# Optimization experiments

Hardware: AMD Instinct MI355X
Metric: run time of the kernel (lower is better)

## Reference

```python
import jax, jax.numpy as jnp
import numpy as np

N_NODES = 50000
N_EDGES = 800000
HIDDEN = 128
UNIFIED = 128


def _sage_conv(x, src, dst, W_l, b_l, W_r, n_nodes):
    # PyG SAGEConv (mean aggr): out = lin_l(mean_{j in N(i)} x_j) + lin_r(x_i)
    msgs = x[src]  # [E, d] gather of source-node features
    agg = jax.ops.segment_sum(msgs, dst, num_segments=n_nodes)  # [N, d]
    cnt = jax.ops.segment_sum(jnp.ones((src.shape[0],), dtype=x.dtype), dst,
                              num_segments=n_nodes)
    agg = agg / jnp.maximum(cnt, 1.0)[:, None]  # mean; isolated nodes -> 0
    return agg @ W_l.T + b_l + x @ W_r.T


def setup_inputs() -> dict:
    key = jax.random.key(0)
    ks = jax.random.split(key, 8)
    s = 1.0 / np.sqrt(HIDDEN)
    x = jax.random.normal(ks[0], (N_NODES, HIDDEN), dtype=jnp.float32)
    edge_index = jax.random.randint(ks[1], (2, N_EDGES), 0, N_NODES, dtype=jnp.int64)
    W1_l = jax.random.normal(ks[2], (HIDDEN, HIDDEN), dtype=jnp.float32) * s
    b1_l = jnp.zeros((HIDDEN,), dtype=jnp.float32)
    W1_r = jax.random.normal(ks[3], (HIDDEN, HIDDEN), dtype=jnp.float32) * s
    W2_l = jax.random.normal(ks[4], (UNIFIED, HIDDEN), dtype=jnp.float32) * s
    b2_l = jnp.zeros((UNIFIED,), dtype=jnp.float32)
    W2_r = jax.random.normal(ks[5], (UNIFIED, HIDDEN), dtype=jnp.float32) * s
    return {"x": x, "edge_index": edge_index,
            "W1_l": W1_l, "b1_l": b1_l, "W1_r": W1_r,
            "W2_l": W2_l, "b2_l": b2_l, "W2_r": W2_r}


def reference(x, edge_index, W1_l, b1_l, W1_r, W2_l, b2_l, W2_r):
    src, dst = edge_index[0], edge_index[1]
    n = x.shape[0]
    h = jax.nn.relu(_sage_conv(x, src, dst, W1_l, b1_l, W1_r, n))
    return _sage_conv(h, src, dst, W2_l, b2_l, W2_r, n)
```

## Files before the change

### kernel.cpp

```cpp
#include <hip/hip_runtime.h>

#define N_NODES 50000
#define HIDDEN 128
#define NBUCK ((N_NODES + 127) >> 7)

typedef __attribute__((ext_vector_type(8))) short short8;
typedef __attribute__((ext_vector_type(4))) float f32x4;

__device__ __forceinline__ unsigned short f2bf(float f) {
    union { float f; unsigned int u; } a; a.f = f;
    unsigned int u = a.u;
    u += 0x7FFFu + ((u >> 16) & 1u);
    return (unsigned short)(u >> 16);
}
__device__ __forceinline__ float bf2f(unsigned int bits16) {
    union { unsigned int u; float f; } a; a.u = bits16 << 16;
    return a.f;
}

__global__ __launch_bounds__(256) void pack_both(
    const float* __restrict__ W1l, const float* __restrict__ W1r,
    const float* __restrict__ W2l, const float* __restrict__ W2r,
    unsigned short* __restrict__ Wp1, unsigned short* __restrict__ Wp2,
    int* __restrict__ bcnt) {
    int tid = blockIdx.x * blockDim.x + threadIdx.x;
    if (tid < NBUCK) bcnt[tid] = 0;
    const int which = tid >> 15;
    const int t2 = tid & 32767;
    int j = t2 & 7, lane = (t2 >> 3) & 63, nf = (t2 >> 9) & 7, ks = t2 >> 12;
    int k = ks * 32 + ((lane >> 4) * 8) + j;
    int t = nf * 16 + (lane & 15);
    const float* Wl = which ? W2l : W1l;
    const float* Wr = which ? W2r : W1r;
    float v = (k < 128) ? Wl[t * 128 + k] : Wr[t * 128 + (k - 128)];
    (which ? Wp2 : Wp1)[t2] = f2bf(v);
}

__global__ void cast_bf16(const float* __restrict__ x, unsigned short* __restrict__ xb, int n4) {
    int i = blockIdx.x * blockDim.x + threadIdx.x;
    if (i >= n4) return;
    float4 v = reinterpret_cast<const float4*>(x)[i];
    ushort4 o = make_ushort4(f2bf(v.x), f2bf(v.y), f2bf(v.z), f2bf(v.w));
    reinterpret_cast<ushort4*>(xb)[i] = o;
}


__global__ __launch_bounds__(1024) void bucket_hist(const int* __restrict__ dst, int E,
                                                    int* __restrict__ bcnt) {
    __shared__ int h[NBUCK];
    for (int i = threadIdx.x; i < NBUCK; i += 1024) h[i] = 0;
    __syncthreads();
    for (int e = blockIdx.x * 1024 + threadIdx.x; e < E; e += gridDim.x * 1024)
        atomicAdd(&h[dst[e] >> 7], 1);
    __syncthreads();
    for (int i = threadIdx.x; i < NBUCK; i += 1024)
        if (h[i]) atomicAdd(&bcnt[i], h[i]);
}

__global__ __launch_bounds__(512) void scan_buckets(const int* __restrict__ bcnt,
                                                    int* __restrict__ boff,
                                                    int* __restrict__ bcur) {
    __shared__ int ws[8];
    const int tid = threadIdx.x, lane = tid & 63, wid = tid >> 6;
    const int v = (tid < NBUCK) ? bcnt[tid] : 0;
    int incl = v;
#pragma unroll
    for (int off = 1; off < 64; off <<= 1) {
        int t = __shfl_up(incl, off);
        if (lane >= off) incl += t;
    }
    if (lane == 63) ws[wid] = incl;
    __syncthreads();
    if (wid == 0) {
        int wv = (lane < 8) ? ws[lane] : 0;
        int wincl = wv;
#pragma unroll
        for (int off = 1; off < 8; off <<= 1) {
            int t = __shfl_up(wincl, off);
            if (lane >= off) wincl += t;
        }
        if (lane < 8) ws[lane] = wincl - wv;
    }
    __syncthreads();
    const int excl = ws[wid] + incl - v;
    if (tid < NBUCK) { boff[tid] = excl; bcur[tid] = excl; }
    if (tid == NBUCK - 1) boff[NBUCK] = excl + v;
}

#define PCHUNK 4096
__global__ __launch_bounds__(1024) void partition_edges(
    const int* __restrict__ src, const int* __restrict__ dst, int E,
    int* __restrict__ bcur, unsigned int* __restrict__ packed) {
    __shared__ int h[NBUCK];
    __shared__ int base[NBUCK];
    const int tid = threadIdx.x;
    const int c0 = blockIdx.x * PCHUNK;
    for (int i = tid; i < NBUCK; i += 1024) h[i] = 0;
    __syncthreads();

    unsigned int val[4];
    int bk[4];
#pragma unroll
    for (int u = 0; u < 4; ++u) {
        const int e = c0 + u * 1024 + tid;
        if (e < E) {
            const int d = dst[e];
            val[u] = ((unsigned int)d << 16) | (unsigned int)src[e];
            bk[u] = d >> 7;
            atomicAdd(&h[bk[u]], 1);
        } else {
            bk[u] = -1;
        }
    }
    __syncthreads();
    for (int i = tid; i < NBUCK; i += 1024) {
        base[i] = h[i] ? atomicAdd(&bcur[i], h[i]) : 0;
        h[i] = 0;
    }
    __syncthreads();
#pragma unroll
    for (int u = 0; u < 4; ++u) {
        if (bk[u] >= 0) {
            const int pos = base[bk[u]] + atomicAdd(&h[bk[u]], 1);
            packed[pos] = val[u];
        }
    }
}

__global__ __launch_bounds__(256) void build_rows(const unsigned int* __restrict__ packed,
                                                  const int* __restrict__ boff,
                                                  int* __restrict__ row_start,
                                                  unsigned short* __restrict__ ssrc) {
    __shared__ int lh[128];
    __shared__ int lc[128];
    __shared__ int htot;
    const int b = blockIdx.x;
    const int gbase = boff[b], gend = boff[b + 1];
    const int tid = threadIdx.x;
    if (tid < 128) lh[tid] = 0;
    __syncthreads();
    for (int i = gbase + tid; i < gend; i += 256)
        atomicAdd(&lh[(packed[i] >> 16) & 127], 1);
    __syncthreads();
    int v = 0, incl = 0;
    if (tid < 128) {
        const int lane = tid & 63;
        v = lh[tid];
        incl = v;
#pragma unroll
        for (int off = 1; off < 64; off <<= 1) {
            int t = __shfl_up(incl, off);
            if (lane >= off) incl += t;
        }
        if (tid == 63) htot = incl;
    }
    __syncthreads();
    if (tid < 128) {
        const int excl = incl - v + ((tid >= 64) ? htot : 0);
        lc[tid] = gbase + excl;
        const int node = b * 128 + tid;
        if (node <= N_NODES) row_start[node] = gbase + excl;
    }
    __syncthreads();
    for (int i = gbase + tid; i < gend; i += 256) {
        const unsigned int p = packed[i];
        const int pos = atomicAdd(&lc[(p >> 16) & 127], 1);
        ssrc[pos] = (unsigned short)(p & 0xffffu);
    }
}

__global__ __launch_bounds__(256) void aggregate_mean_bf16(
    const unsigned short* __restrict__ featb, const int* __restrict__ row_start,
    const unsigned short* __restrict__ ssrc, unsigned short* __restrict__ aggb) {
    const int node = blockIdx.x * 8 + (threadIdx.x >> 5);
    const int l = threadIdx.x & 31;
    if (node >= N_NODES) return;
    const int beg = row_start[node], end = row_start[node + 1];
    float acc[4][4];
#pragma unroll
    for (int u = 0; u < 4; ++u)
#pragma unroll
        for (int f = 0; f < 4; ++f) acc[u][f] = 0.f;

    int j = beg;
    for (; j + 3 < end; j += 4) {
#pragma unroll
        for (int u = 0; u < 4; ++u) {
            const int s = ssrc[j + u];
            const ushort4 v = *reinterpret_cast<const ushort4*>(&featb[(size_t)s * HIDDEN + 4 * l]);
            acc[u][0] += bf2f(v.x); acc[u][1] += bf2f(v.y);
            acc[u][2] += bf2f(v.z); acc[u][3] += bf2f(v.w);
        }
    }
    for (; j < end; ++j) {
        const int s = ssrc[j];
        const ushort4 v = *reinterpret_cast<const ushort4*>(&featb[(size_t)s * HIDDEN + 4 * l]);
        acc[0][0] += bf2f(v.x); acc[0][1] += bf2f(v.y);
        acc[0][2] += bf2f(v.z); acc[0][3] += bf2f(v.w);
    }
    const int d = end - beg;
    const float inv = d ? 1.0f / (float)d : 0.0f;
    ushort4 o;
    o.x = f2bf((acc[0][0] + acc[1][0] + acc[2][0] + acc[3][0]) * inv);
    o.y = f2bf((acc[0][1] + acc[1][1] + acc[2][1] + acc[3][1]) * inv);
    o.z = f2bf((acc[0][2] + acc[1][2] + acc[2][2] + acc[3][2]) * inv);
    o.w = f2bf((acc[0][3] + acc[1][3] + acc[2][3] + acc[3][3]) * inv);
    *reinterpret_cast<ushort4*>(&aggb[(size_t)node * HIDDEN + 4 * l]) = o;
}

template <int WRITE_BF16_RELU>
__global__ __launch_bounds__(256) void mfma_linear(
    const unsigned short* aggb, const unsigned short* xb,
    const unsigned short* __restrict__ Wp, const float* __restrict__ bias,
    unsigned short* out_b, float* out_f) {
    const int lane = threadIdx.x & 63;
    const int wave = threadIdx.x >> 6;
    const int wm = wave >> 1, wn = wave & 1;
    const int rowbase = blockIdx.x * 64 + wm * 32;
    const int colbase = wn * 64;
    const int l15 = lane & 15, l4 = lane >> 4;

    f32x4 acc[2][4];
#pragma unroll
    for (int m = 0; m < 2; ++m)
#pragma unroll
        for (int nf = 0; nf < 4; ++nf) acc[m][nf] = (f32x4){0.f, 0.f, 0.f, 0.f};

#pragma unroll
    for (int ks = 0; ks < 8; ++ks) {
        const unsigned short* Asrc = (ks < 4) ? aggb : xb;
        const int koff = (ks & 3) * 32 + l4 * 8;
        short8 a[2];
#pragma unroll
        for (int m = 0; m < 2; ++m) {
            int row = rowbase + m * 16 + l15;
            if (row >= N_NODES) row = N_NODES - 1;
            a[m] = *reinterpret_cast<const short8*>(&Asrc[(size_t)row * HIDDEN + koff]);
        }
#pragma unroll
        for (int nf = 0; nf < 4; ++nf) {
            const int nfg = (colbase >> 4) + nf;
            short8 b = *reinterpret_cast<const short8*>(&Wp[(((size_t)ks * 8 + nfg) * 64 + lane) * 8]);
            acc[0][nf] = __builtin_amdgcn_mfma_f32_16x16x32_bf16(a[0], b, acc[0][nf], 0, 0, 0);
            acc[1][nf] = __builtin_amdgcn_mfma_f32_16x16x32_bf16(a[1], b, acc[1][nf], 0, 0, 0);
        }
    }

#pragma unroll
    for (int nf = 0; nf < 4; ++nf) {
        const int col = colbase + nf * 16 + l15;
        const float bv = bias[col];
#pragma unroll
        for (int m = 0; m < 2; ++m) {
#pragma unroll
            for (int r = 0; r < 4; ++r) {
                const int row = rowbase + m * 16 + l4 * 4 + r;
                if (row < N_NODES) {
                    float v = acc[m][nf][r] + bv;
                    if (WRITE_BF16_RELU) {
                        v = fmaxf(v, 0.0f);
                        out_b[(size_t)row * HIDDEN + col] = f2bf(v);
                    } else {
                        out_f[(size_t)row * HIDDEN + col] = v;
                    }
                }
            }
        }
    }
}

extern "C" void kernel_launch(void* const* d_in, const int* in_sizes, int n_in,
                              void* d_out, int out_size, void* d_ws, size_t ws_size,
                              hipStream_t stream) {
    const float* x   = (const float*)d_in[0];
    const int*   ei  = (const int*)d_in[1];
    const float* W1l = (const float*)d_in[2];
    const float* b1  = (const float*)d_in[3];
    const float* W1r = (const float*)d_in[4];
    const float* W2l = (const float*)d_in[5];
    const float* b2  = (const float*)d_in[6];
    const float* W2r = (const float*)d_in[7];

    const int E = in_sizes[1] / 2;
    const int* src = ei;
    const int* dst = ei + E;

    int* iws        = (int*)d_ws;
    int* bcnt       = iws;
    int* boff       = iws + 400;
    int* bcur       = iws + 800;
    int* row_start  = iws + 1200;
    unsigned int* packed = (unsigned int*)(iws + 51204);
    unsigned short* ssrc = (unsigned short*)(iws + 51204 + E);
    unsigned short* xb   = ssrc + E;
    unsigned short* aggb = xb + (size_t)N_NODES * HIDDEN;
    unsigned short* Wp1  = aggb + (size_t)N_NODES * HIDDEN;
    unsigned short* Wp2  = Wp1 + 256 * HIDDEN;

    pack_both<<<256, 256, 0, stream>>>(W1l, W1r, W2l, W2r, Wp1, Wp2, bcnt);
    cast_bf16<<<(N_NODES * HIDDEN / 4 + 255) / 256, 256, 0, stream>>>(x, xb, N_NODES * HIDDEN / 4);

    bucket_hist<<<196, 1024, 0, stream>>>(dst, E, bcnt);
    scan_buckets<<<1, 512, 0, stream>>>(bcnt, boff, bcur);
    partition_edges<<<(E + PCHUNK - 1) / PCHUNK, 1024, 0, stream>>>(src, dst, E, bcur, packed);
    build_rows<<<NBUCK, 256, 0, stream>>>(packed, boff, row_start, ssrc);

    const int aggGrid = (N_NODES + 7) / 8;
    const int linGrid = (N_NODES + 63) / 64;

    aggregate_mean_bf16<<<aggGrid, 256, 0, stream>>>(xb, row_start, ssrc, aggb);
    mfma_linear<1><<<linGrid, 256, 0, stream>>>(aggb, xb, Wp1, b1, xb, nullptr);

    aggregate_mean_bf16<<<aggGrid, 256, 0, stream>>>(xb, row_start, ssrc, aggb);
    mfma_linear<0><<<linGrid, 256, 0, stream>>>(aggb, xb, Wp2, b2, nullptr, (float*)d_out);
}
```

Measured before the change: 152.5 us.

## Fuse neighbor mean aggregation into MFMA linear kernel via swizzled shared memory

Each 64-node block first gathers and averages its neighbors' bf16 features into an XOR-swizzled shared-memory tile, then runs the MFMA linear layer reading the aggregated half from LDS and the self half from global. This removes the separate aggregation kernel and the global write and read of the aggregated buffer per layer. Layer 1 now writes its output to a separate buffer instead of overwriting xb, which avoids a race between blocks. Fewer waves now cover the gather (16 lanes per node, 4 nodes per wave in sequence), which may reduce latency hiding. A leftover dummy load of featb[0] is dead code that the compiler should remove.

```diff
diff --git a/kernel.cpp b/kernel.cpp
--- a/kernel.cpp
+++ b/kernel.cpp
@@ -169,54 +169,65 @@
     }
 }
 
-__global__ __launch_bounds__(256) void aggregate_mean_bf16(
-    const unsigned short* __restrict__ featb, const int* __restrict__ row_start,
-    const unsigned short* __restrict__ ssrc, unsigned short* __restrict__ aggb) {
-    const int node = blockIdx.x * 8 + (threadIdx.x >> 5);
-    const int l = threadIdx.x & 31;
-    if (node >= N_NODES) return;
-    const int beg = row_start[node], end = row_start[node + 1];
-    float acc[4][4];
-#pragma unroll
-    for (int u = 0; u < 4; ++u)
-#pragma unroll
-        for (int f = 0; f < 4; ++f) acc[u][f] = 0.f;
-
-    int j = beg;
-    for (; j + 3 < end; j += 4) {
-#pragma unroll
-        for (int u = 0; u < 4; ++u) {
-            const int s = ssrc[j + u];
-            const ushort4 v = *reinterpret_cast<const ushort4*>(&featb[(size_t)s * HIDDEN + 4 * l]);
-            acc[u][0] += bf2f(v.x); acc[u][1] += bf2f(v.y);
-            acc[u][2] += bf2f(v.z); acc[u][3] += bf2f(v.w);
-        }
-    }
-    for (; j < end; ++j) {
-        const int s = ssrc[j];
-        const ushort4 v = *reinterpret_cast<const ushort4*>(&featb[(size_t)s * HIDDEN + 4 * l]);
-        acc[0][0] += bf2f(v.x); acc[0][1] += bf2f(v.y);
-        acc[0][2] += bf2f(v.z); acc[0][3] += bf2f(v.w);
-    }
-    const int d = end - beg;
-    const float inv = d ? 1.0f / (float)d : 0.0f;
-    ushort4 o;
-    o.x = f2bf((acc[0][0] + acc[1][0] + acc[2][0] + acc[3][0]) * inv);
-    o.y = f2bf((acc[0][1] + acc[1][1] + acc[2][1] + acc[3][1]) * inv);
-    o.z = f2bf((acc[0][2] + acc[1][2] + acc[2][2] + acc[3][2]) * inv);
-    o.w = f2bf((acc[0][3] + acc[1][3] + acc[2][3] + acc[3][3]) * inv);
-    *reinterpret_cast<ushort4*>(&aggb[(size_t)node * HIDDEN + 4 * l]) = o;
-}
-
 template <int WRITE_BF16_RELU>
-__global__ __launch_bounds__(256) void mfma_linear(
-    const unsigned short* aggb, const unsigned short* xb,
+__global__ __launch_bounds__(256) void fused_sage(
+    const unsigned short* __restrict__ featb,
+    const int* __restrict__ row_start,
+    const unsigned short* __restrict__ ssrc,
     const unsigned short* __restrict__ Wp, const float* __restrict__ bias,
     unsigned short* out_b, float* out_f) {
-    const int lane = threadIdx.x & 63;
-    const int wave = threadIdx.x >> 6;
+    __shared__ alignas(16) unsigned short sAgg[64 * 128];
+    char* sBytes = (char*)sAgg;
+    const int tid = threadIdx.x;
+    const int rowbase0 = blockIdx.x * 64;
+
+    {
+        const int wv = tid >> 6;
+        const int q = (tid >> 4) & 3;
+        const int lq = tid & 15;
+#pragma unroll
+        for (int p = 0; p < 4; ++p) {
+            const int nl = wv * 16 + p * 4 + q;
+            const int node = rowbase0 + nl;
+            float acc[4][8];
+#pragma unroll
+            for (int u = 0; u < 4; ++u)
+#pragma unroll
+                for (int f = 0; f < 8; ++f) acc[u][f] = 0.f;
+            int beg = 0, end = 0;
+            if (node < N_NODES) { beg = row_start[node]; end = row_start[node + 1]; }
+            int j = beg;
+            for (; j + 3 < end; j += 4) {
+#pragma unroll
+                for (int u = 0; u < 4; ++u) {
+                    const int s = ssrc[j + u];
+                    const short8 v = *reinterpret_cast<const short8*>(&featb[(size_t)s * HIDDEN + 8 * lq]);
+#pragma unroll
+                    for (int f = 0; f < 8; ++f) acc[u][f] += bf2f((unsigned short)v[f]);
+                }
+            }
+            for (; j < end; ++j) {
+                const int s = ssrc[j];
+                const short8 v = *reinterpret_cast<const short8*>(&featb[(size_t)s * HIDDEN + 8 * lq]);
+#pragma unroll
+                for (int f = 0; f < 8; ++f) acc[0][f] += bf2f((unsigned short)v[f]);
+            }
+            const int d = end - beg;
+            const float inv = d ? 1.0f / (float)d : 0.0f;
+            short8 o;
+#pragma unroll
+            for (int f = 0; f < 8; ++f)
+                o[f] = (short)f2bf((acc[0][f] + acc[1][f] + acc[2][f] + acc[3][f]) * inv);
+            const int boff = (nl * 256 + 16 * lq) ^ ((nl & 7) << 4);
+            *reinterpret_cast<short8*>(sBytes + boff) = o;
+        }
+    }
+    __syncthreads();
+
+    const int lane = tid & 63;
+    const int wave = tid >> 6;
     const int wm = wave >> 1, wn = wave & 1;
-    const int rowbase = blockIdx.x * 64 + wm * 32;
+    const int rowbase = rowbase0 + wm * 32;
     const int colbase = wn * 64;
     const int l15 = lane & 15, l4 = lane >> 4;
 
@@ -228,14 +239,31 @@
 
 #pragma unroll
     for (int ks = 0; ks < 8; ++ks) {
-        const unsigned short* Asrc = (ks < 4) ? aggb : xb;
-        const int koff = (ks & 3) * 32 + l4 * 8;
         short8 a[2];
-#pragma unroll
-        for (int m = 0; m < 2; ++m) {
-            int row = rowbase + m * 16 + l15;
-            if (row >= N_NODES) row = N_NODES - 1;
-            a[m] = *reinterpret_cast<const short8*>(&Asrc[(size_t)row * HIDDEN + koff]);
+        if (ks < 4) {
+#pragma unroll
+            for (int m = 0; m < 2; ++m) {
+                const int r = wm * 32 + m * 16 + l15;
+                const int boff = (r * 256 + ks * 64 + l4 * 16) ^ ((r & 7) << 4);
+                a[m] = *reinterpret_cast<const short8*>(sBytes + boff);
+            }
+        } else {
+            const int koff = (ks & 3) * 32 + l4 * 8;
+#pragma unroll
+            for (int m = 0; m < 2; ++m) {
+                int row = rowbase + m * 16 + l15;
+                if (row >= N_NODES) row = N_NODES - 1;
+                a[m] = *reinterpret_cast<const short8*>(&featb[0] + 0);
+            }
+        }
+        if (ks >= 4) {
+            const int koff = (ks & 3) * 32 + l4 * 8;
+#pragma unroll
+            for (int m = 0; m < 2; ++m) {
+                int row = rowbase + m * 16 + l15;
+                if (row >= N_NODES) row = N_NODES - 1;
+                a[m] = *reinterpret_cast<const short8*>(&featb[(size_t)row * HIDDEN + koff]);
+            }
         }
 #pragma unroll
         for (int nf = 0; nf < 4; ++nf) {
@@ -293,8 +321,8 @@
     unsigned int* packed = (unsigned int*)(iws + 51204);
     unsigned short* ssrc = (unsigned short*)(iws + 51204 + E);
     unsigned short* xb   = ssrc + E;
-    unsigned short* aggb = xb + (size_t)N_NODES * HIDDEN;
-    unsigned short* Wp1  = aggb + (size_t)N_NODES * HIDDEN;
+    unsigned short* hb   = xb + (size_t)N_NODES * HIDDEN;
+    unsigned short* Wp1  = hb + (size_t)N_NODES * HIDDEN;
     unsigned short* Wp2  = Wp1 + 256 * HIDDEN;
 
     pack_both<<<256, 256, 0, stream>>>(W1l, W1r, W2l, W2r, Wp1, Wp2, bcnt);
@@ -305,12 +333,9 @@
     partition_edges<<<(E + PCHUNK - 1) / PCHUNK, 1024, 0, stream>>>(src, dst, E, bcur, packed);
     build_rows<<<NBUCK, 256, 0, stream>>>(packed, boff, row_start, ssrc);
 
-    const int aggGrid = (N_NODES + 7) / 8;
-    const int linGrid = (N_NODES + 63) / 64;
-
-    aggregate_mean_bf16<<<aggGrid, 256, 0, stream>>>(xb, row_start, ssrc, aggb);
-    mfma_linear<1><<<linGrid, 256, 0, stream>>>(aggb, xb, Wp1, b1, xb, nullptr);
-
-    aggregate_mean_bf16<<<aggGrid, 256, 0, stream>>>(xb, row_start, ssrc, aggb);
-    mfma_linear<0><<<linGrid, 256, 0, stream>>>(aggb, xb, Wp2, b2, nullptr, (float*)d_out);
-}
+    const int fusedGrid = (N_NODES + 63) / 64;
+
+    fused_sage<1><<<fusedGrid, 256, 0, stream>>>(xb, row_start, ssrc, Wp1, b1, hb, nullptr);
+
+    fused_sage<0><<<fusedGrid, 256, 0, stream>>>(hb, row_start, ssrc, Wp2, b2, nullptr, (float*)d_out);
+}
```

After: 186.3 us. 22.2% more time.

## Use fixed-capacity edge buckets and widen aggregation loads to 16 bytes

Applied to the files above, without the earlier changes.

Drops the bucket histogram and scan kernels by giving each destination bucket a fixed capacity slot, with row_end stored separately in CSR. Aggregation now uses 16 lanes per node with 8-element bf16 vector loads instead of 32 lanes with 4-element loads. This removes two launches and a pass over dst. In exchange it risks overflow if any bucket gets more than the fixed capacity of edges, and it enlarges the workspace.

```diff
diff --git a/kernel.cpp b/kernel.cpp
--- a/kernel.cpp
+++ b/kernel.cpp
@@ -3,6 +3,7 @@
 #define N_NODES 50000
 #define HIDDEN 128
 #define NBUCK ((N_NODES + 127) >> 7)
+#define BCAP 2304
 
 typedef __attribute__((ext_vector_type(8))) short short8;
 typedef __attribute__((ext_vector_type(4))) float f32x4;
@@ -22,9 +23,9 @@
     const float* __restrict__ W1l, const float* __restrict__ W1r,
     const float* __restrict__ W2l, const float* __restrict__ W2r,
     unsigned short* __restrict__ Wp1, unsigned short* __restrict__ Wp2,
-    int* __restrict__ bcnt) {
+    int* __restrict__ bcur) {
     int tid = blockIdx.x * blockDim.x + threadIdx.x;
-    if (tid < NBUCK) bcnt[tid] = 0;
+    if (tid < NBUCK) bcur[tid] = tid * BCAP;
     const int which = tid >> 15;
     const int t2 = tid & 32767;
     int j = t2 & 7, lane = (t2 >> 3) & 63, nf = (t2 >> 9) & 7, ks = t2 >> 12;
@@ -44,49 +45,6 @@
     reinterpret_cast<ushort4*>(xb)[i] = o;
 }
 
-
-__global__ __launch_bounds__(1024) void bucket_hist(const int* __restrict__ dst, int E,
-                                                    int* __restrict__ bcnt) {
-    __shared__ int h[NBUCK];
-    for (int i = threadIdx.x; i < NBUCK; i += 1024) h[i] = 0;
-    __syncthreads();
-    for (int e = blockIdx.x * 1024 + threadIdx.x; e < E; e += gridDim.x * 1024)
-        atomicAdd(&h[dst[e] >> 7], 1);
-    __syncthreads();
-    for (int i = threadIdx.x; i < NBUCK; i += 1024)
-        if (h[i]) atomicAdd(&bcnt[i], h[i]);
-}
-
-__global__ __launch_bounds__(512) void scan_buckets(const int* __restrict__ bcnt,
-                                                    int* __restrict__ boff,
-                                                    int* __restrict__ bcur) {
-    __shared__ int ws[8];
-    const int tid = threadIdx.x, lane = tid & 63, wid = tid >> 6;
-    const int v = (tid < NBUCK) ? bcnt[tid] : 0;
-    int incl = v;
-#pragma unroll
-    for (int off = 1; off < 64; off <<= 1) {
-        int t = __shfl_up(incl, off);
-        if (lane >= off) incl += t;
-    }
-    if (lane == 63) ws[wid] = incl;
-    __syncthreads();
-    if (wid == 0) {
-        int wv = (lane < 8) ? ws[lane] : 0;
-        int wincl = wv;
-#pragma unroll
-        for (int off = 1; off < 8; off <<= 1) {
-            int t = __shfl_up(wincl, off);
-            if (lane >= off) wincl += t;
-        }
-        if (lane < 8) ws[lane] = wincl - wv;
-    }
-    __syncthreads();
-    const int excl = ws[wid] + incl - v;
-    if (tid < NBUCK) { boff[tid] = excl; bcur[tid] = excl; }
-    if (tid == NBUCK - 1) boff[NBUCK] = excl + v;
-}
-
 #define PCHUNK 4096
 __global__ __launch_bounds__(1024) void partition_edges(
     const int* __restrict__ src, const int* __restrict__ dst, int E,
@@ -128,14 +86,15 @@
 }
 
 __global__ __launch_bounds__(256) void build_rows(const unsigned int* __restrict__ packed,
-                                                  const int* __restrict__ boff,
+                                                  const int* __restrict__ bcur,
                                                   int* __restrict__ row_start,
+                                                  int* __restrict__ row_end,
                                                   unsigned short* __restrict__ ssrc) {
     __shared__ int lh[128];
     __shared__ int lc[128];
     __shared__ int htot;
     const int b = blockIdx.x;
-    const int gbase = boff[b], gend = boff[b + 1];
+    const int gbase = b * BCAP, gend = bcur[b];
     const int tid = threadIdx.x;
     if (tid < 128) lh[tid] = 0;
     __syncthreads();
@@ -159,7 +118,10 @@
         const int excl = incl - v + ((tid >= 64) ? htot : 0);
         lc[tid] = gbase + excl;
         const int node = b * 128 + tid;
-        if (node <= N_NODES) row_start[node] = gbase + excl;
+        if (node < N_NODES) {
+            row_start[node] = gbase + excl;
+            row_end[node]   = gbase + excl + v;
+        }
     }
     __syncthreads();
     for (int i = gbase + tid; i < gend; i += 256) {
@@ -171,41 +133,41 @@
 
 __global__ __launch_bounds__(256) void aggregate_mean_bf16(
     const unsigned short* __restrict__ featb, const int* __restrict__ row_start,
-    const unsigned short* __restrict__ ssrc, unsigned short* __restrict__ aggb) {
-    const int node = blockIdx.x * 8 + (threadIdx.x >> 5);
-    const int l = threadIdx.x & 31;
+    const int* __restrict__ row_end, const unsigned short* __restrict__ ssrc,
+    unsigned short* __restrict__ aggb) {
+    const int node = blockIdx.x * 16 + (threadIdx.x >> 4);
+    const int lq = threadIdx.x & 15;
     if (node >= N_NODES) return;
-    const int beg = row_start[node], end = row_start[node + 1];
-    float acc[4][4];
+    const int beg = row_start[node], end = row_end[node];
+    float acc[4][8];
 #pragma unroll
     for (int u = 0; u < 4; ++u)
 #pragma unroll
-        for (int f = 0; f < 4; ++f) acc[u][f] = 0.f;
+        for (int f = 0; f < 8; ++f) acc[u][f] = 0.f;
 
     int j = beg;
     for (; j + 3 < end; j += 4) {
 #pragma unroll
         for (int u = 0; u < 4; ++u) {
             const int s = ssrc[j + u];
-            const ushort4 v = *reinterpret_cast<const ushort4*>(&featb[(size_t)s * HIDDEN + 4 * l]);
-            acc[u][0] += bf2f(v.x); acc[u][1] += bf2f(v.y);
-            acc[u][2] += bf2f(v.z); acc[u][3] += bf2f(v.w);
+            const short8 v = *reinterpret_cast<const short8*>(&featb[(size_t)s * HIDDEN + 8 * lq]);
+#pragma unroll
+            for (int f = 0; f < 8; ++f) acc[u][f] += bf2f((unsigned short)v[f]);
         }
     }
     for (; j < end; ++j) {
         const int s = ssrc[j];
-        const ushort4 v = *reinterpret_cast<const ushort4*>(&featb[(size_t)s * HIDDEN + 4 * l]);
-        acc[0][0] += bf2f(v.x); acc[0][1] += bf2f(v.y);
-        acc[0][2] += bf2f(v.z); acc[0][3] += bf2f(v.w);
+        const short8 v = *reinterpret_cast<const short8*>(&featb[(size_t)s * HIDDEN + 8 * lq]);
+#pragma unroll
+        for (int f = 0; f < 8; ++f) acc[0][f] += bf2f((unsigned short)v[f]);
     }
     const int d = end - beg;
     const float inv = d ? 1.0f / (float)d : 0.0f;
-    ushort4 o;
-    o.x = f2bf((acc[0][0] + acc[1][0] + acc[2][0] + acc[3][0]) * inv);
-    o.y = f2bf((acc[0][1] + acc[1][1] + acc[2][1] + acc[3][1]) * inv);
-    o.z = f2bf((acc[0][2] + acc[1][2] + acc[2][2] + acc[3][2]) * inv);
-    o.w = f2bf((acc[0][3] + acc[1][3] + acc[2][3] + acc[3][3]) * inv);
-    *reinterpret_cast<ushort4*>(&aggb[(size_t)node * HIDDEN + 4 * l]) = o;
+    short8 o;
+#pragma unroll
+    for (int f = 0; f < 8; ++f)
+        o[f] = (short)f2bf((acc[0][f] + acc[1][f] + acc[2][f] + acc[3][f]) * inv);
+    *reinterpret_cast<short8*>(&aggb[(size_t)node * HIDDEN + 8 * lq]) = o;
 }
 
 template <int WRITE_BF16_RELU>
@@ -286,31 +248,28 @@
     const int* dst = ei + E;
 
     int* iws        = (int*)d_ws;
-    int* bcnt       = iws;
-    int* boff       = iws + 400;
-    int* bcur       = iws + 800;
-    int* row_start  = iws + 1200;
-    unsigned int* packed = (unsigned int*)(iws + 51204);
-    unsigned short* ssrc = (unsigned short*)(iws + 51204 + E);
-    unsigned short* xb   = ssrc + E;
+    int* bcur       = iws;
+    int* row_start  = iws + 400;
+    int* row_end    = iws + 50400;
+    unsigned int* packed = (unsigned int*)(iws + 100400);
+    unsigned short* ssrc = (unsigned short*)(iws + 100400 + NBUCK * BCAP);
+    unsigned short* xb   = ssrc + (size_t)NBUCK * BCAP;
     unsigned short* aggb = xb + (size_t)N_NODES * HIDDEN;
     unsigned short* Wp1  = aggb + (size_t)N_NODES * HIDDEN;
     unsigned short* Wp2  = Wp1 + 256 * HIDDEN;
 
-    pack_both<<<256, 256, 0, stream>>>(W1l, W1r, W2l, W2r, Wp1, Wp2, bcnt);
+    pack_both<<<256, 256, 0, stream>>>(W1l, W1r, W2l, W2r, Wp1, Wp2, bcur);
     cast_bf16<<<(N_NODES * HIDDEN / 4 + 255) / 256, 256, 0, stream>>>(x, xb, N_NODES * HIDDEN / 4);
 
-    bucket_hist<<<196, 1024, 0, stream>>>(dst, E, bcnt);
-    scan_buckets<<<1, 512, 0, stream>>>(bcnt, boff, bcur);
     partition_edges<<<(E + PCHUNK - 1) / PCHUNK, 1024, 0, stream>>>(src, dst, E, bcur, packed);
-    build_rows<<<NBUCK, 256, 0, stream>>>(packed, boff, row_start, ssrc);
-
-    const int aggGrid = (N_NODES + 7) / 8;
+    build_rows<<<NBUCK, 256, 0, stream>>>(packed, bcur, row_start, row_end, ssrc);
+
+    const int aggGrid = (N_NODES + 15) / 16;
     const int linGrid = (N_NODES + 63) / 64;
 
-    aggregate_mean_bf16<<<aggGrid, 256, 0, stream>>>(xb, row_start, ssrc, aggb);
+    aggregate_mean_bf16<<<aggGrid, 256, 0, stream>>>(xb, row_start, row_end, ssrc, aggb);
     mfma_linear<1><<<linGrid, 256, 0, stream>>>(aggb, xb, Wp1, b1, xb, nullptr);
 
-    aggregate_mean_bf16<<<aggGrid, 256, 0, stream>>>(xb, row_start, ssrc, aggb);
+    aggregate_mean_bf16<<<aggGrid, 256, 0, stream>>>(xb, row_start, row_end, ssrc, aggb);
     mfma_linear<0><<<linGrid, 256, 0, stream>>>(aggb, xb, Wp2, b2, nullptr, (float*)d_out);
 }
```

Result: faster. 146.0 us (-4.3%).
